# Performance work log

Hardware: AMD Instinct MI355X
Metric: run time of the kernel (lower is better)

Reference implementation:

```python
import jax, jax.numpy as jnp
import numpy as np

# Config (matches init_kwargs)
B, T_IN, N, F_IN = 64, 12, 500, 2
N_RES, N_DIL, N_SKIP, N_END = 64, 64, 256, 512
K_SIZE, N_BLOCKS, N_LAYERS = 2, 4, 2
EDGE_DIM, N_PRED, N_OUT = 2, 12, 1
RECEPTIVE = N_BLOCKS * (K_SIZE - 1) * (2 ** N_LAYERS - 1) + 1  # 13
DILS = [2 ** i for _ in range(N_BLOCKS) for i in range(N_LAYERS)]  # [1,2,1,2,1,2,1,2]
L = len(DILS)
BN_EPS = 1e-5


def setup_inputs() -> dict:
    key = jax.random.key(0)
    ks = jax.random.split(key, 20)
    inputs = jax.random.normal(ks[0], (B, T_IN, N, F_IN), dtype=jnp.float32)
    u = jax.random.uniform(ks[1], (EDGE_DIM, N, N), dtype=jnp.float32)
    supports = u / u.sum(-1, keepdims=True)  # row-stochastic diffusion matrices
    def w(k, shape, fan_in):
        return jax.random.normal(k, shape, dtype=jnp.float32) * (1.0 / np.sqrt(fan_in))
    return {
        "inputs": inputs,
        "supports": supports,
        "enter_w": w(ks[2], (N_RES, F_IN), F_IN),
        "enter_b": jnp.zeros((N_RES,), jnp.float32),
        "filter_w": w(ks[3], (L, N_DIL, N_RES, 1, K_SIZE), N_RES * K_SIZE),
        "filter_b": jnp.zeros((L, N_DIL), jnp.float32),
        "gate_w": w(ks[4], (L, N_DIL, N_RES, 1, K_SIZE), N_RES * K_SIZE),
        "gate_b": jnp.zeros((L, N_DIL), jnp.float32),
        "gconv_w": w(ks[5], (L, N_RES, EDGE_DIM * N_DIL), EDGE_DIM * N_DIL),
        "gconv_b": jnp.zeros((L, N_RES), jnp.float32),
        "skip_w": w(ks[6], (L, N_SKIP, N_DIL), N_DIL),
        "skip_b": jnp.zeros((L, N_SKIP), jnp.float32),
        "bn_gamma": jnp.ones((L, N_RES), jnp.float32),
        "bn_beta": jnp.zeros((L, N_RES), jnp.float32),
        "out1_w": w(ks[7], (N_END, N_SKIP), N_SKIP),
        "out1_b": jnp.zeros((N_END,), jnp.float32),
        "out2_w": w(ks[8], (N_PRED * N_OUT, N_END), N_END),
        "out2_b": jnp.zeros((N_PRED * N_OUT,), jnp.float32),
    }


def _conv_t(x, w, b, dil):
    # x: [B,C,N,T], w: [O,I,1,k] dilated along time, VALID padding
    y = jax.lax.conv_general_dilated(x, w, window_strides=(1, 1), padding="VALID",
                                     rhs_dilation=(1, dil),
                                     dimension_numbers=("NCHW", "OIHW", "NCHW"))
    return y + b[None, :, None, None]


def _forward(inputs, supports, enter_w, enter_b, filter_w, filter_b, gate_w, gate_b,
             gconv_w, gconv_b, skip_w, skip_b, bn_gamma, bn_beta,
             out1_w, out1_b, out2_w, out2_b):
    x = jnp.transpose(inputs, (0, 3, 2, 1))  # [B,F,N,T]
    pad = RECEPTIVE - x.shape[3]
    if pad > 0:
        x = jnp.pad(x, ((0, 0), (0, 0), (0, 0), (pad, 0)))
    x = jnp.einsum("of,bfnt->bont", enter_w, x) + enter_b[None, :, None, None]
    b = x.shape[0]
    skip = jnp.zeros((b, N_SKIP, N, x.shape[3]), jnp.float32)
    for i, d in enumerate(DILS):
        residual = x
        f = jnp.tanh(_conv_t(residual, filter_w[i], filter_b[i], d))
        g = jax.nn.sigmoid(_conv_t(residual, gate_w[i], gate_b[i], d))
        x = f * g  # [B, n_dil, N, t']
        s = jnp.einsum("oc,bcnt->bont", skip_w[i], x) + skip_b[i][None, :, None, None]
        skip = skip[..., -s.shape[3]:] + s
        # graph diffusion conv: propagate over each support, mix channels
        h = jnp.einsum("knm,bcmt->bkcnt", supports, x)
        bb, kk, cc, nn, tt = h.shape
        h = h.reshape(bb, kk * cc, nn, tt)
        x = jnp.einsum("oi,bint->bont", gconv_w[i], h) + gconv_b[i][None, :, None, None]
        # dropout is identity in eval mode
        x = x + residual[..., -x.shape[3]:]
        # BatchNorm2d (training-mode batch statistics)
        mean = x.mean(axis=(0, 2, 3), keepdims=True)
        var = ((x - mean) ** 2).mean(axis=(0, 2, 3), keepdims=True)
        x = (x - mean) * jax.lax.rsqrt(var + BN_EPS)
        x = x * bn_gamma[i][None, :, None, None] + bn_beta[i][None, :, None, None]
    y = jax.nn.relu(skip)  # [B, n_skips, N, 1]
    y = jax.nn.relu(jnp.einsum("os,bsnt->bont", out1_w, y) + out1_b[None, :, None, None])
    y = jnp.einsum("oe,bent->bont", out2_w, y) + out2_b[None, :, None, None]
    # [B, n_pred*n_out, N, 1] -> [B, n_pred, N, n_out]
    y = y.reshape(b, N_PRED, -1, N)
    return jnp.swapaxes(y, -1, -2)


def reference(inputs, supports, enter_w, enter_b, filter_w, filter_b, gate_w, gate_b,
              gconv_w, gconv_b, skip_w, skip_b, bn_gamma, bn_beta,
              out1_w, out1_b, out2_w, out2_b):
    return _forward(inputs, supports, enter_w, enter_b, filter_w, filter_b, gate_w, gate_b,
                    gconv_w, gconv_b, skip_w, skip_b, bn_gamma, bn_beta,
                    out1_w, out1_b, out2_w, out2_b)
```

## Files before the change

kernel.cpp:

```cpp
#include <hip/hip_runtime.h>

typedef float v4 __attribute__((ext_vector_type(4)));
typedef short bf8 __attribute__((ext_vector_type(8)));
typedef unsigned short u16;
typedef unsigned int u32;

#define DEVI __device__ __forceinline__

namespace {

constexpr int B = 64, C = 64, NPT = 500, NP = 512, T0 = 13, SC = 256, EC = 512, PR = 12;
constexpr size_t SLOTP = (size_t)B * C * NP;

constexpr size_t SZ_BUF  = 13 * SLOTP * 2;
constexpr size_t OFF_SK  = 2 * SZ_BUF;
constexpr size_t SZ_SK   = (size_t)SC * B * NPT * 4;
constexpr size_t OFF_ST  = OFF_SK + SZ_SK;
constexpr size_t OFF_STP = OFF_ST + 1024;
constexpr size_t OFF_W1T = OFF_STP + 1024;
constexpr size_t OFF_WMX = OFF_W1T + (size_t)131072*4;
constexpr size_t OFF_WFB = OFF_WMX + (size_t)65536*2;
constexpr size_t OFF_WGB = OFF_WFB + (size_t)65536*2;
constexpr size_t OFF_SWB = OFF_WGB + (size_t)65536*2;
constexpr size_t OFF_SPD = OFF_SWB + (size_t)131072*2;
constexpr size_t OFF_PSUM = OFF_SPD + (size_t)524288*2;
constexpr size_t WS_NEED = OFF_PSUM + (size_t)768*128*4;

DEVI float sigm(float x) { return 1.f / (1.f + expf(-x)); }
DEVI float bf2f(u16 u) { u32 x = ((u32)u) << 16; float f; __builtin_memcpy(&f, &x, 4); return f; }
DEVI u16 f2bf(float f) { u32 x; __builtin_memcpy(&x, &f, 4); return (u16)((x + 0x7FFF + ((x >> 16) & 1)) >> 16); }
DEVI int swzA(int n, int k) { int byte = (n << 8) + (k << 1); byte ^= (((n >> 1) ^ (n >> 3)) & 7) << 4; return byte; }
DEVI int swzS(int n, int cp) { int byte = (n << 7) + (cp << 1); byte ^= (((n >> 1) ^ (n >> 3)) & 7) << 4; return byte; }
DEVI int swzX(int r, int c) { int byte = (r << 10) + (c << 1); byte ^= (r & 7) << 4; return byte; }
DEVI int swzG(int n, int k) { int byte = (n << 7) + (k << 1); byte ^= (n & 7) << 4; return byte; }

__global__ void k_debug_ws(float* __restrict__ out, float val) {
  int i = blockIdx.x * 256 + threadIdx.x;
  if (i < B * PR * NPT) out[i] = val;
}

__global__ void k_prep(const float* __restrict__ fw, const float* __restrict__ gw,
                       const float* __restrict__ sw, const float* __restrict__ gcw,
                       const float* __restrict__ o1w, const float* __restrict__ sup,
                       u16* __restrict__ WFB, u16* __restrict__ WGB,
                       u16* __restrict__ SWB, u16* __restrict__ WMX,
                       float* __restrict__ W1T, u16* __restrict__ SPD,
                       float* __restrict__ STP) {
  int i = blockIdx.x * 256 + threadIdx.x;
  if (i < 65536) {
    int k = i & 127, cp = (i >> 7) & 63, l = i >> 13;
    int tap = k >> 6, c = k & 63;
    int g = ((l * 64 + cp) * 64 + c) * 2 + tap;
    WFB[i] = f2bf(fw[g]);
    WGB[i] = f2bf(gw[g]);
  }
  int j = i - 65536;
  if (j >= 0 && j < 131072) {
    int c = j & 63, o = (j >> 6) & 255, l = j >> 14;
    SWB[j] = f2bf(sw[(l * 256 + o) * 64 + c]);
  }
  int k2 = i - 196608;
  if (k2 >= 0 && k2 < 65536) WMX[k2] = f2bf(gcw[k2]);
  int m = i - 262144;
  if (m >= 0 && m < 131072) {
    int e = m & 511, o = m >> 9;
    W1T[m] = o1w[e * 256 + o];
  }
  int sp = i - 393216;
  if (sp >= 0 && sp < 524288) {
    int mm = sp & 511, n = (sp >> 9) & 511, s = sp >> 18;
    float v = (n < NPT && mm < NPT) ? sup[(size_t)s * NPT * NPT + (size_t)n * NPT + mm] : 0.f;
    SPD[sp] = f2bf(v);
  }
  int q = i - 917504;
  if (q >= 0 && q < 192) STP[q] = (q >= 64 && q < 128) ? 1.f : 0.f;
}

__global__ void k_enter(const float* __restrict__ in, const float* __restrict__ ew,
                        const float* __restrict__ eb, u16* __restrict__ X) {
  size_t idx = (size_t)blockIdx.x * 256 + threadIdx.x;
  if (idx >= 13 * SLOTP) return;
  int t = (int)(idx / SLOTP);
  size_t r = idx % SLOTP;
  int n = (int)(r % NP);
  int c = (int)((r / NP) % C);
  int b = (int)(r / ((size_t)NP * C));
  float v = 0.f;
  if (n < NPT) {
    v = eb[c];
    if (t > 0) {
      const float* ip = in + (((size_t)b * 12 + (t - 1)) * NPT + n) * 2;
      v += ew[c * 2] * ip[0] + ew[c * 2 + 1] * ip[1];
    }
  }
  X[idx] = f2bf(v);
}

__global__ void k_zero_sk(float* __restrict__ p) {
  size_t i = ((size_t)blockIdx.x * 256 + threadIdx.x) * 4;
  v4 z = {};
  *(v4*)&p[i] = z;
}

__global__ __launch_bounds__(1024) void k_gatedconv(
    const u16* __restrict__ X, u16* __restrict__ XA,
    const float* __restrict__ STP,
    const u16* __restrict__ WFl, const float* __restrict__ bfb,
    const u16* __restrict__ WGl, const float* __restrict__ bgb,
    const u16* __restrict__ SWl, const float* __restrict__ sb,
    float* __restrict__ SK, int d, int Tp) {
  __shared__ u16 L[65536];
  const int lane = threadIdx.x, w = threadIdx.y;
  const int tid = w * 64 + lane;
  const int t = blockIdx.x, b = blockIdx.y;
  const int lrow = lane & 15, kgrp = lane >> 4;
  const int nbase = w * 32;

  for (int i = tid; i < 8192; i += 1024) {
    int tap = i >> 12;
    int c = (i >> 6) & 63;
    int n0 = (i & 63) * 8;
    const u16* src = &X[(size_t)(t + tap * d) * SLOTP + ((size_t)b * C + c) * NP + n0];
    float mean = STP[c], scl = STP[64 + c], sh = STP[128 + c];
    ushort4 a = *(const ushort4*)src;
    ushort4 a2 = *(const ushort4*)(src + 4);
    u16 vals[8] = {a.x, a.y, a.z, a.w, a2.x, a2.y, a2.z, a2.w};
    int k = tap * 64 + c;
#pragma unroll
    for (int jj = 0; jj < 8; ++jj) {
      int n = n0 + jj;
      L[swzA(n, k) >> 1] = f2bf((bf2f(vals[jj]) - mean) * scl + sh);
    }
  }
  __syncthreads();

  v4 af[2][4], ag[2][4];
#pragma unroll
  for (int a1 = 0; a1 < 2; ++a1)
#pragma unroll
    for (int a2 = 0; a2 < 4; ++a2) { af[a1][a2] = (v4){0.f,0.f,0.f,0.f}; ag[a1][a2] = (v4){0.f,0.f,0.f,0.f}; }

#pragma unroll
  for (int k0 = 0; k0 < 128; k0 += 32) {
    const int kof = k0 + kgrp * 8;
    bf8 Av[2];
#pragma unroll
    for (int nt = 0; nt < 2; ++nt) {
      int n = nbase + nt * 16 + lrow;
      Av[nt] = *(const bf8*)&L[swzA(n, kof) >> 1];
    }
#pragma unroll
    for (int ct = 0; ct < 4; ++ct) {
      bf8 Fw = *(const bf8*)&WFl[(size_t)(ct * 16 + lrow) * 128 + kof];
      bf8 Gw = *(const bf8*)&WGl[(size_t)(ct * 16 + lrow) * 128 + kof];
#pragma unroll
      for (int nt = 0; nt < 2; ++nt) {
        af[nt][ct] = __builtin_amdgcn_mfma_f32_16x16x32_bf16(Av[nt], Fw, af[nt][ct], 0, 0, 0);
        ag[nt][ct] = __builtin_amdgcn_mfma_f32_16x16x32_bf16(Av[nt], Gw, ag[nt][ct], 0, 0, 0);
      }
    }
  }

  const size_t xab = (size_t)t * SLOTP + (size_t)b * C * NP;
  ushort4 ovv[2][4];
#pragma unroll
  for (int nt = 0; nt < 2; ++nt) {
    int n0s = nbase + nt * 16 + kgrp * 4;
#pragma unroll
    for (int ct = 0; ct < 4; ++ct) {
      int cp = ct * 16 + lrow;
      float fb = bfb[cp], gb2 = bgb[cp];
      ushort4 ov;
      ov.x = f2bf(tanhf(af[nt][ct][0] + fb) * sigm(ag[nt][ct][0] + gb2));
      ov.y = f2bf(tanhf(af[nt][ct][1] + fb) * sigm(ag[nt][ct][1] + gb2));
      ov.z = f2bf(tanhf(af[nt][ct][2] + fb) * sigm(ag[nt][ct][2] + gb2));
      ov.w = f2bf(tanhf(af[nt][ct][3] + fb) * sigm(ag[nt][ct][3] + gb2));
      ovv[nt][ct] = ov;
      if (n0s < NPT) *(ushort4*)&XA[xab + (size_t)cp * NP + n0s] = ov;
    }
  }

  if (t == Tp - 1) {
    __syncthreads();
#pragma unroll
    for (int nt = 0; nt < 2; ++nt) {
      int n0s = nbase + nt * 16 + kgrp * 4;
#pragma unroll
      for (int ct = 0; ct < 4; ++ct) {
        int cp = ct * 16 + lrow;
        ushort4 ov = ovv[nt][ct];
        L[swzS(n0s + 0, cp) >> 1] = ov.x;
        L[swzS(n0s + 1, cp) >> 1] = ov.y;
        L[swzS(n0s + 2, cp) >> 1] = ov.z;
        L[swzS(n0s + 3, cp) >> 1] = ov.w;
      }
    }
    __syncthreads();
#pragma unroll 1
    for (int ot = 0; ot < 16; ++ot) {
      v4 a[2];
#pragma unroll
      for (int nt = 0; nt < 2; ++nt) a[nt] = (v4){0.f,0.f,0.f,0.f};
#pragma unroll
      for (int k0 = 0; k0 < 64; k0 += 32) {
        const int kof = k0 + kgrp * 8;
        bf8 Bs = *(const bf8*)&SWl[(size_t)(ot * 16 + lrow) * 64 + kof];
#pragma unroll
        for (int nt = 0; nt < 2; ++nt) {
          int n = nbase + nt * 16 + lrow;
          bf8 Av2 = *(const bf8*)&L[swzS(n, kof) >> 1];
          a[nt] = __builtin_amdgcn_mfma_f32_16x16x32_bf16(Av2, Bs, a[nt], 0, 0, 0);
        }
      }
      int o = ot * 16 + lrow;
      float bb = sb[o];
#pragma unroll
      for (int nt = 0; nt < 2; ++nt) {
        int n0s = nbase + nt * 16 + kgrp * 4;
        if (n0s < NPT) {
          float* dst = &SK[(size_t)o * (B * NPT) + (size_t)b * NPT + n0s];
          v4 old = *(const v4*)dst;
          *(v4*)dst = old + a[nt] + bb;
        }
      }
    }
  }
}

__global__ __launch_bounds__(512) void k_diffmix(
    const u16* __restrict__ XA, const u16* __restrict__ XIN, u16* __restrict__ XOUT,
    const u16* __restrict__ SPD, const u16* __restrict__ WMXl,
    const float* __restrict__ gb, const float* __restrict__ STP,
    float* __restrict__ PSUM, int d) {
  __shared__ u16 SH[65536];
  __shared__ float sst[128];
  u16* XS = SH;
  u16* GS = SH + 32768;
  const int lane = threadIdx.x;
  const int w = threadIdx.y;
  const int tid = w * 64 + lane;
  const int t = blockIdx.x, b = blockIdx.y;
  const int lrow = lane & 15;
  const int kgrp = lane >> 4;
  const int nbase = w * 64;
  const size_t xabase = ((size_t)t * (B * C) + (size_t)b * C) * NP;
  if (tid < 128) sst[tid] = 0.f;

  for (int i = tid; i < 4096; i += 512) {
    int c = i >> 6, slot = i & 63;
    const u16* src = &XA[xabase + (size_t)c * NP + slot * 8];
    ushort4 a0 = *(const ushort4*)src;
    ushort4 a1 = *(const ushort4*)(src + 4);
    int byte = swzX(c, slot * 8);
    *(ushort4*)&XS[byte >> 1] = a0;
    *(ushort4*)&XS[(byte >> 1) + 4] = a1;
  }
  __syncthreads();

  v4 acc2[4][4];
#pragma unroll
  for (int a = 0; a < 4; ++a)
#pragma unroll
    for (int c2 = 0; c2 < 4; ++c2) acc2[a][c2] = (v4){0.f, 0.f, 0.f, 0.f};

#pragma unroll 1
  for (int s = 0; s < 2; ++s) {
    v4 acc[4][4];
#pragma unroll
    for (int a = 0; a < 4; ++a)
#pragma unroll
      for (int c2 = 0; c2 < 4; ++c2) acc[a][c2] = (v4){0.f, 0.f, 0.f, 0.f};
    const u16* Sb = SPD + (size_t)s * (512 * 512);
    bf8 Ac[4];
#pragma unroll
    for (int nt = 0; nt < 4; ++nt)
      Ac[nt] = *(const bf8*)&Sb[(size_t)(nbase + nt * 16 + lrow) * 512 + kgrp * 8];
#pragma unroll 1
    for (int k0 = 0; k0 < 512; k0 += 32) {
      const int kof = k0 + kgrp * 8;
      bf8 An[4];
      if (k0 + 32 < 512) {
#pragma unroll
        for (int nt = 0; nt < 4; ++nt)
          An[nt] = *(const bf8*)&Sb[(size_t)(nbase + nt * 16 + lrow) * 512 + kof + 32];
      }
      bf8 Bf[4];
#pragma unroll
      for (int ct = 0; ct < 4; ++ct)
        Bf[ct] = *(const bf8*)&XS[swzX(ct * 16 + lrow, kof) >> 1];
#pragma unroll
      for (int nt = 0; nt < 4; ++nt)
#pragma unroll
        for (int ct = 0; ct < 4; ++ct)
          acc[nt][ct] = __builtin_amdgcn_mfma_f32_16x16x32_bf16(Ac[nt], Bf[ct], acc[nt][ct], 0, 0, 0);
#pragma unroll
      for (int nt = 0; nt < 4; ++nt) Ac[nt] = An[nt];
    }
#pragma unroll
    for (int nt = 0; nt < 4; ++nt)
#pragma unroll
      for (int ct = 0; ct < 4; ++ct)
#pragma unroll
        for (int r = 0; r < 4; ++r) {
          int n = nbase + nt * 16 + kgrp * 4 + r;
          int k = ct * 16 + lrow;
          GS[swzG(n, k) >> 1] = f2bf(acc[nt][ct][r]);
        }
    __syncthreads();
#pragma unroll
    for (int k0 = 0; k0 < 64; k0 += 32) {
      const int kof = k0 + kgrp * 8;
      bf8 Af[4], Bw[4];
#pragma unroll
      for (int nt = 0; nt < 4; ++nt)
        Af[nt] = *(const bf8*)&GS[swzG(nbase + nt * 16 + lrow, kof) >> 1];
#pragma unroll
      for (int ot = 0; ot < 4; ++ot)
        Bw[ot] = *(const bf8*)&WMXl[(size_t)(ot * 16 + lrow) * 128 + s * 64 + kof];
#pragma unroll
      for (int nt = 0; nt < 4; ++nt)
#pragma unroll
        for (int ot = 0; ot < 4; ++ot)
          acc2[nt][ot] = __builtin_amdgcn_mfma_f32_16x16x32_bf16(Af[nt], Bw[ot], acc2[nt][ot], 0, 0, 0);
    }
    __syncthreads();
  }

#pragma unroll
  for (int nt = 0; nt < 4; ++nt) {
    int n0 = nbase + nt * 16 + kgrp * 4;
#pragma unroll
    for (int ot = 0; ot < 4; ++ot) {
      int o = ot * 16 + lrow;
      int byte = swzX(o, n0);
      ushort4 gv;
      gv.x = f2bf(acc2[nt][ot][0]);
      gv.y = f2bf(acc2[nt][ot][1]);
      gv.z = f2bf(acc2[nt][ot][2]);
      gv.w = f2bf(acc2[nt][ot][3]);
      *(ushort4*)&XS[byte >> 1] = gv;
    }
  }
  __syncthreads();
  const size_t rbase = ((size_t)(t + d) * (B * C) + (size_t)b * C) * NP;
#pragma unroll 1
  for (int i = 0; i < 8; ++i) {
    int idx = i * 512 + tid;
    int o = idx >> 6;
    int ck = idx & 63;
    int byte = swzX(o, ck * 8);
    ushort4 g0 = *(const ushort4*)&XS[byte >> 1];
    ushort4 g1 = *(const ushort4*)&XS[(byte >> 1) + 4];
    int n0 = ck * 8;
    const u16* rp = &XIN[rbase + (size_t)o * NP + n0];
    ushort4 r0 = *(const ushort4*)rp;
    ushort4 r1 = *(const ushort4*)(rp + 4);
    float m = STP[o], sc = STP[64 + o], h = STP[128 + o];
    float bias = gb[o];
    float v[8];
    v[0] = bf2f(g0.x) + bias + (bf2f(r0.x) - m) * sc + h;
    v[1] = bf2f(g0.y) + bias + (bf2f(r0.y) - m) * sc + h;
    v[2] = bf2f(g0.z) + bias + (bf2f(r0.z) - m) * sc + h;
    v[3] = bf2f(g0.w) + bias + (bf2f(r0.w) - m) * sc + h;
    v[4] = bf2f(g1.x) + bias + (bf2f(r1.x) - m) * sc + h;
    v[5] = bf2f(g1.y) + bias + (bf2f(r1.y) - m) * sc + h;
    v[6] = bf2f(g1.z) + bias + (bf2f(r1.z) - m) * sc + h;
    v[7] = bf2f(g1.w) + bias + (bf2f(r1.w) - m) * sc + h;
    ushort4 s0, s1;
    s0.x = f2bf(v[0]); s0.y = f2bf(v[1]); s0.z = f2bf(v[2]); s0.w = f2bf(v[3]);
    s1.x = f2bf(v[4]); s1.y = f2bf(v[5]); s1.z = f2bf(v[6]); s1.w = f2bf(v[7]);
    u16* op = &XOUT[xabase + (size_t)o * NP + n0];
    *(ushort4*)op = s0;
    *(ushort4*)(op + 4) = s1;
    float ls = 0.f, lq = 0.f;
#pragma unroll
    for (int e = 0; e < 8; ++e)
      if (n0 + e < NPT) { ls += v[e]; lq += v[e] * v[e]; }
#pragma unroll
    for (int off = 32; off; off >>= 1) {
      ls += __shfl_down(ls, off, 64);
      lq += __shfl_down(lq, off, 64);
    }
    if (lane == 0) {
      atomicAdd(&sst[o], ls);
      atomicAdd(&sst[64 + o], lq);
    }
  }
  __syncthreads();
  if (tid < 128) PSUM[(size_t)(blockIdx.y * gridDim.x + blockIdx.x) * 128 + tid] = sst[tid];
}

__global__ __launch_bounds__(1024) void k_bnfin(
    const float* __restrict__ PSUM, float* __restrict__ stp,
    const float* __restrict__ gamma, const float* __restrict__ beta,
    int nblk, int Tp) {
  __shared__ double red[1024];
  int tid = threadIdx.x;
  int c = tid & 127;
  int ch = tid >> 7;
  double s = 0.0;
  for (int r = ch; r < nblk; r += 8) s += (double)PSUM[(size_t)r * 128 + c];
  red[tid] = s;
  __syncthreads();
  if (ch < 4) red[tid] += red[tid + 512];
  __syncthreads();
  if (ch < 2) red[tid] += red[tid + 256];
  __syncthreads();
  if (ch == 0) red[c] = red[c] + red[c + 128];
  __syncthreads();
  if (tid < 64) {
    double cnt = (double)Tp * (double)(B * NPT);
    double m = red[tid] / cnt;
    double v = red[64 + tid] / cnt - m * m;
    stp[tid] = (float)m;
    stp[64 + tid] = gamma[tid] * rsqrtf((float)v + 1e-5f);
    stp[128 + tid] = beta[tid];
  }
}

__global__ __launch_bounds__(256) void k_out1(const float* __restrict__ SK,
                                              const float* __restrict__ W1T,
                                              const float* __restrict__ b1,
                                              u16* __restrict__ H1) {
  __shared__ __align__(16) float ssm[32 * 64];
  __shared__ __align__(16) float wsm[32 * 64];
  const int tx = threadIdx.x, ty = threadIdx.y;
  const int tid = ty * 16 + tx;
  const int p0 = blockIdx.x * 64, e0 = blockIdx.y * 64;
  v4 acc[4] = {};
  for (int o0 = 0; o0 < SC; o0 += 32) {
    __syncthreads();
    for (int i = tid; i < 2048; i += 256) {
      int pp = i & 63, kk = i >> 6;
      ssm[i] = fmaxf(SK[(size_t)(o0 + kk) * (B * NPT) + p0 + pp], 0.f);
      wsm[i] = W1T[(size_t)(o0 + kk) * 512 + e0 + pp];
    }
    __syncthreads();
#pragma unroll
    for (int kk = 0; kk < 32; ++kk) {
      v4 sv = *(const v4*)&ssm[kk * 64 + tx * 4];
      v4 wv = *(const v4*)&wsm[kk * 64 + ty * 4];
#pragma unroll
      for (int r = 0; r < 4; ++r) acc[r] += wv[r] * sv;
    }
  }
#pragma unroll
  for (int r = 0; r < 4; ++r) {
    int e = e0 + ty * 4 + r;
    float bb = b1[e];
    size_t ob = (size_t)e * (B * NPT) + p0 + tx * 4;
#pragma unroll
    for (int q = 0; q < 4; ++q) H1[ob + q] = f2bf(fmaxf(acc[r][q] + bb, 0.f));
  }
}

__global__ __launch_bounds__(256) void k_out2(const u16* __restrict__ H1,
                                              const float* __restrict__ W2,
                                              const float* __restrict__ b2,
                                              float* __restrict__ out) {
  int idx = blockIdx.x * 256 + threadIdx.x;
  if (idx >= B * PR * NPT) return;
  int n = idx % NPT;
  int p12 = (idx / NPT) % PR;
  int b = idx / (NPT * PR);
  size_t p = (size_t)b * NPT + n;
  const float* w = W2 + p12 * EC;
  float acc = b2[p12];
  for (int e = 0; e < EC; e += 4) {
    acc += w[e] * bf2f(H1[(size_t)e * (B * NPT) + p])
         + w[e + 1] * bf2f(H1[(size_t)(e + 1) * (B * NPT) + p])
         + w[e + 2] * bf2f(H1[(size_t)(e + 2) * (B * NPT) + p])
         + w[e + 3] * bf2f(H1[(size_t)(e + 3) * (B * NPT) + p]);
  }
  out[idx] = acc;
}

}

extern "C" void kernel_launch(void* const* d_in, const int* in_sizes, int n_in,
                              void* d_out, int out_size, void* d_ws, size_t ws_size,
                              hipStream_t stream) {
  const float* inputs  = (const float*)d_in[0];
  const float* sup     = (const float*)d_in[1];
  const float* enter_w = (const float*)d_in[2];
  const float* enter_b = (const float*)d_in[3];
  const float* filt_w  = (const float*)d_in[4];
  const float* filt_b  = (const float*)d_in[5];
  const float* gate_w  = (const float*)d_in[6];
  const float* gate_b  = (const float*)d_in[7];
  const float* gconv_w = (const float*)d_in[8];
  const float* gconv_b = (const float*)d_in[9];
  const float* skip_w  = (const float*)d_in[10];
  const float* skip_b  = (const float*)d_in[11];
  const float* bn_g    = (const float*)d_in[12];
  const float* bn_b    = (const float*)d_in[13];
  const float* o1w     = (const float*)d_in[14];
  const float* o1b     = (const float*)d_in[15];
  const float* o2w     = (const float*)d_in[16];
  const float* o2b     = (const float*)d_in[17];
  (void)in_sizes; (void)n_in; (void)out_size;

  if (ws_size < WS_NEED) {
    k_debug_ws<<<1500, 256, 0, stream>>>((float*)d_out, (float)(ws_size >> 20));
    return;
  }

  char* base = (char*)d_ws;
  u16*    buf0 = (u16*)base;
  u16*    buf1 = (u16*)(base + SZ_BUF);
  float*  SK   = (float*)(base + OFF_SK);
  float*  STP  = (float*)(base + OFF_STP);
  float*  W1T  = (float*)(base + OFF_W1T);
  u16*    WMX  = (u16*)(base + OFF_WMX);
  u16*    WFB  = (u16*)(base + OFF_WFB);
  u16*    WGB  = (u16*)(base + OFF_WGB);
  u16*    SWB  = (u16*)(base + OFF_SWB);
  u16*    SPD  = (u16*)(base + OFF_SPD);
  float*  PSUM = (float*)(base + OFF_PSUM);

  k_prep<<<3586, 256, 0, stream>>>(filt_w, gate_w, skip_w, gconv_w, o1w, sup,
                                   WFB, WGB, SWB, WMX, W1T, SPD, STP);
  k_enter<<<(int)((13 * SLOTP) / 256), 256, 0, stream>>>(inputs, enter_w, enter_b, buf0);
  k_zero_sk<<<8000, 256, 0, stream>>>(SK);

  static const int dils[8] = {1, 2, 1, 2, 1, 2, 1, 2};
  u16* bufs[2] = {buf0, buf1};
  int T = T0;
  for (int l = 0; l < 8; ++l) {
    const int d = dils[l];
    const int Tp = T - d;
    u16* XIN = bufs[l & 1];
    u16* XAb = bufs[(l + 1) & 1];
    k_gatedconv<<<dim3(Tp, B), dim3(64, 16), 0, stream>>>(
        XIN, XAb, STP, WFB + l * 8192, filt_b + l * 64, WGB + l * 8192, gate_b + l * 64,
        SWB + l * 16384, skip_b + l * 256, SK, d, Tp);
    if (l < 7) {
      k_diffmix<<<dim3(Tp, B), dim3(64, 8), 0, stream>>>(
          XAb, XIN, XAb, SPD, WMX + l * 8192, gconv_b + l * 64, STP, PSUM, d);
      k_bnfin<<<1, 1024, 0, stream>>>(PSUM, STP, bn_g + l * 64, bn_b + l * 64, Tp * B, Tp);
    }
    T = Tp;
  }

  u16* H1 = buf1;
  k_out1<<<dim3(500, 8), dim3(16, 16), 0, stream>>>(SK, W1T, o1b, H1);
  k_out2<<<1500, 256, 0, stream>>>(H1, o2w, o2b, (float*)d_out);
}
```

Measured before the change: 2.138 ms.

## Fuse gated conv into diffusion-mix kernel, fold BatchNorm into next layer weights

```diff
diff --git a/kernel.cpp b/kernel.cpp
--- a/kernel.cpp
+++ b/kernel.cpp
@@ -24,13 +24,15 @@
 constexpr size_t OFF_SWB = OFF_WGB + (size_t)65536*2;
 constexpr size_t OFF_SPD = OFF_SWB + (size_t)131072*2;
 constexpr size_t OFF_PSUM = OFF_SPD + (size_t)524288*2;
-constexpr size_t WS_NEED = OFF_PSUM + (size_t)768*128*4;
+constexpr size_t OFF_WFP = OFF_PSUM + (size_t)768*128*4;
+constexpr size_t OFF_WGP = OFF_WFP + 16384;
+constexpr size_t OFF_BFP = OFF_WGP + 16384;
+constexpr size_t OFF_BGP = OFF_BFP + 256;
+constexpr size_t WS_NEED = OFF_BGP + 256;
 
 DEVI float sigm(float x) { return 1.f / (1.f + expf(-x)); }
 DEVI float bf2f(u16 u) { u32 x = ((u32)u) << 16; float f; __builtin_memcpy(&f, &x, 4); return f; }
 DEVI u16 f2bf(float f) { u32 x; __builtin_memcpy(&x, &f, 4); return (u16)((x + 0x7FFF + ((x >> 16) & 1)) >> 16); }
-DEVI int swzA(int n, int k) { int byte = (n << 8) + (k << 1); byte ^= (((n >> 1) ^ (n >> 3)) & 7) << 4; return byte; }
-DEVI int swzS(int n, int cp) { int byte = (n << 7) + (cp << 1); byte ^= (((n >> 1) ^ (n >> 3)) & 7) << 4; return byte; }
 DEVI int swzX(int r, int c) { int byte = (r << 10) + (c << 1); byte ^= (r & 7) << 4; return byte; }
 DEVI int swzG(int n, int k) { int byte = (n << 7) + (k << 1); byte ^= (n & 7) << 4; return byte; }
 
@@ -42,10 +44,13 @@
 __global__ void k_prep(const float* __restrict__ fw, const float* __restrict__ gw,
                        const float* __restrict__ sw, const float* __restrict__ gcw,
                        const float* __restrict__ o1w, const float* __restrict__ sup,
+                       const float* __restrict__ fbias, const float* __restrict__ gbias,
                        u16* __restrict__ WFB, u16* __restrict__ WGB,
                        u16* __restrict__ SWB, u16* __restrict__ WMX,
                        float* __restrict__ W1T, u16* __restrict__ SPD,
-                       float* __restrict__ STP) {
+                       float* __restrict__ STP,
+                       u16* __restrict__ WFP, u16* __restrict__ WGP,
+                       float* __restrict__ BFP, float* __restrict__ BGP) {
   int i = blockIdx.x * 256 + threadIdx.x;
   if (i < 65536) {
     int k = i & 127, cp = (i >> 7) & 63, l = i >> 13;
@@ -74,6 +79,19 @@
   }
   int q = i - 917504;
   if (q >= 0 && q < 192) STP[q] = (q >= 64 && q < 128) ? 1.f : 0.f;
+  int w0 = i - 917696;
+  if (w0 >= 0 && w0 < 8192) {
+    int k = w0 & 127, cp = w0 >> 7;
+    int tap = k >> 6, c = k & 63;
+    int g = (cp * 64 + c) * 2 + tap;
+    WFP[w0] = f2bf(fw[g]);
+    WGP[w0] = f2bf(gw[g]);
+  }
+  int b0 = i - 925888;
+  if (b0 >= 0 && b0 < 128) {
+    if (b0 < 64) BFP[b0] = fbias[b0];
+    else BGP[b0 - 64] = gbias[b0 - 64];
+  }
 }
 
 __global__ void k_enter(const float* __restrict__ in, const float* __restrict__ ew,
@@ -82,9 +100,9 @@
   if (idx >= 13 * SLOTP) return;
   int t = (int)(idx / SLOTP);
   size_t r = idx % SLOTP;
-  int n = (int)(r % NP);
-  int c = (int)((r / NP) % C);
-  int b = (int)(r / ((size_t)NP * C));
+  int c = (int)(r & 63);
+  int n = (int)((r >> 6) & 511);
+  int b = (int)(r >> 15);
   float v = 0.f;
   if (n < NPT) {
     v = eb[c];
@@ -102,136 +120,15 @@
   *(v4*)&p[i] = z;
 }
 
-__global__ __launch_bounds__(1024) void k_gatedconv(
-    const u16* __restrict__ X, u16* __restrict__ XA,
-    const float* __restrict__ STP,
-    const u16* __restrict__ WFl, const float* __restrict__ bfb,
-    const u16* __restrict__ WGl, const float* __restrict__ bgb,
-    const u16* __restrict__ SWl, const float* __restrict__ sb,
-    float* __restrict__ SK, int d, int Tp) {
-  __shared__ u16 L[65536];
-  const int lane = threadIdx.x, w = threadIdx.y;
-  const int tid = w * 64 + lane;
-  const int t = blockIdx.x, b = blockIdx.y;
-  const int lrow = lane & 15, kgrp = lane >> 4;
-  const int nbase = w * 32;
-
-  for (int i = tid; i < 8192; i += 1024) {
-    int tap = i >> 12;
-    int c = (i >> 6) & 63;
-    int n0 = (i & 63) * 8;
-    const u16* src = &X[(size_t)(t + tap * d) * SLOTP + ((size_t)b * C + c) * NP + n0];
-    float mean = STP[c], scl = STP[64 + c], sh = STP[128 + c];
-    ushort4 a = *(const ushort4*)src;
-    ushort4 a2 = *(const ushort4*)(src + 4);
-    u16 vals[8] = {a.x, a.y, a.z, a.w, a2.x, a2.y, a2.z, a2.w};
-    int k = tap * 64 + c;
-#pragma unroll
-    for (int jj = 0; jj < 8; ++jj) {
-      int n = n0 + jj;
-      L[swzA(n, k) >> 1] = f2bf((bf2f(vals[jj]) - mean) * scl + sh);
-    }
-  }
-  __syncthreads();
-
-  v4 af[2][4], ag[2][4];
-#pragma unroll
-  for (int a1 = 0; a1 < 2; ++a1)
-#pragma unroll
-    for (int a2 = 0; a2 < 4; ++a2) { af[a1][a2] = (v4){0.f,0.f,0.f,0.f}; ag[a1][a2] = (v4){0.f,0.f,0.f,0.f}; }
-
-#pragma unroll
-  for (int k0 = 0; k0 < 128; k0 += 32) {
-    const int kof = k0 + kgrp * 8;
-    bf8 Av[2];
-#pragma unroll
-    for (int nt = 0; nt < 2; ++nt) {
-      int n = nbase + nt * 16 + lrow;
-      Av[nt] = *(const bf8*)&L[swzA(n, kof) >> 1];
-    }
-#pragma unroll
-    for (int ct = 0; ct < 4; ++ct) {
-      bf8 Fw = *(const bf8*)&WFl[(size_t)(ct * 16 + lrow) * 128 + kof];
-      bf8 Gw = *(const bf8*)&WGl[(size_t)(ct * 16 + lrow) * 128 + kof];
-#pragma unroll
-      for (int nt = 0; nt < 2; ++nt) {
-        af[nt][ct] = __builtin_amdgcn_mfma_f32_16x16x32_bf16(Av[nt], Fw, af[nt][ct], 0, 0, 0);
-        ag[nt][ct] = __builtin_amdgcn_mfma_f32_16x16x32_bf16(Av[nt], Gw, ag[nt][ct], 0, 0, 0);
-      }
-    }
-  }
-
-  const size_t xab = (size_t)t * SLOTP + (size_t)b * C * NP;
-  ushort4 ovv[2][4];
-#pragma unroll
-  for (int nt = 0; nt < 2; ++nt) {
-    int n0s = nbase + nt * 16 + kgrp * 4;
-#pragma unroll
-    for (int ct = 0; ct < 4; ++ct) {
-      int cp = ct * 16 + lrow;
-      float fb = bfb[cp], gb2 = bgb[cp];
-      ushort4 ov;
-      ov.x = f2bf(tanhf(af[nt][ct][0] + fb) * sigm(ag[nt][ct][0] + gb2));
-      ov.y = f2bf(tanhf(af[nt][ct][1] + fb) * sigm(ag[nt][ct][1] + gb2));
-      ov.z = f2bf(tanhf(af[nt][ct][2] + fb) * sigm(ag[nt][ct][2] + gb2));
-      ov.w = f2bf(tanhf(af[nt][ct][3] + fb) * sigm(ag[nt][ct][3] + gb2));
-      ovv[nt][ct] = ov;
-      if (n0s < NPT) *(ushort4*)&XA[xab + (size_t)cp * NP + n0s] = ov;
-    }
-  }
-
-  if (t == Tp - 1) {
-    __syncthreads();
-#pragma unroll
-    for (int nt = 0; nt < 2; ++nt) {
-      int n0s = nbase + nt * 16 + kgrp * 4;
-#pragma unroll
-      for (int ct = 0; ct < 4; ++ct) {
-        int cp = ct * 16 + lrow;
-        ushort4 ov = ovv[nt][ct];
-        L[swzS(n0s + 0, cp) >> 1] = ov.x;
-        L[swzS(n0s + 1, cp) >> 1] = ov.y;
-        L[swzS(n0s + 2, cp) >> 1] = ov.z;
-        L[swzS(n0s + 3, cp) >> 1] = ov.w;
-      }
-    }
-    __syncthreads();
-#pragma unroll 1
-    for (int ot = 0; ot < 16; ++ot) {
-      v4 a[2];
-#pragma unroll
-      for (int nt = 0; nt < 2; ++nt) a[nt] = (v4){0.f,0.f,0.f,0.f};
-#pragma unroll
-      for (int k0 = 0; k0 < 64; k0 += 32) {
-        const int kof = k0 + kgrp * 8;
-        bf8 Bs = *(const bf8*)&SWl[(size_t)(ot * 16 + lrow) * 64 + kof];
-#pragma unroll
-        for (int nt = 0; nt < 2; ++nt) {
-          int n = nbase + nt * 16 + lrow;
-          bf8 Av2 = *(const bf8*)&L[swzS(n, kof) >> 1];
-          a[nt] = __builtin_amdgcn_mfma_f32_16x16x32_bf16(Av2, Bs, a[nt], 0, 0, 0);
-        }
-      }
-      int o = ot * 16 + lrow;
-      float bb = sb[o];
-#pragma unroll
-      for (int nt = 0; nt < 2; ++nt) {
-        int n0s = nbase + nt * 16 + kgrp * 4;
-        if (n0s < NPT) {
-          float* dst = &SK[(size_t)o * (B * NPT) + (size_t)b * NPT + n0s];
-          v4 old = *(const v4*)dst;
-          *(v4*)dst = old + a[nt] + bb;
-        }
-      }
-    }
-  }
-}
-
-__global__ __launch_bounds__(512) void k_diffmix(
-    const u16* __restrict__ XA, const u16* __restrict__ XIN, u16* __restrict__ XOUT,
-    const u16* __restrict__ SPD, const u16* __restrict__ WMXl,
-    const float* __restrict__ gb, const float* __restrict__ STP,
-    float* __restrict__ PSUM, int d) {
+__global__ __launch_bounds__(512) void k_fused(
+    const u16* __restrict__ XIN, u16* __restrict__ XOUT,
+    const u16* __restrict__ SPD,
+    const u16* __restrict__ WFP, const float* __restrict__ BFP,
+    const u16* __restrict__ WGP, const float* __restrict__ BGP,
+    const u16* __restrict__ SWl, const float* __restrict__ sb, float* __restrict__ SK,
+    const u16* __restrict__ WMXl, const float* __restrict__ gb,
+    const float* __restrict__ STP, float* __restrict__ PSUM,
+    int d, int Tp, int dodiff) {
   __shared__ u16 SH[65536];
   __shared__ float sst[128];
   u16* XS = SH;
@@ -243,19 +140,95 @@
   const int lrow = lane & 15;
   const int kgrp = lane >> 4;
   const int nbase = w * 64;
-  const size_t xabase = ((size_t)t * (B * C) + (size_t)b * C) * NP;
+  const size_t x_t  = (size_t)t * SLOTP + (size_t)b * NP * C;
+  const size_t x_td = (size_t)(t + d) * SLOTP + (size_t)b * NP * C;
   if (tid < 128) sst[tid] = 0.f;
 
-  for (int i = tid; i < 4096; i += 512) {
-    int c = i >> 6, slot = i & 63;
-    const u16* src = &XA[xabase + (size_t)c * NP + slot * 8];
-    ushort4 a0 = *(const ushort4*)src;
-    ushort4 a1 = *(const ushort4*)(src + 4);
-    int byte = swzX(c, slot * 8);
-    *(ushort4*)&XS[byte >> 1] = a0;
-    *(ushort4*)&XS[(byte >> 1) + 4] = a1;
-  }
-  __syncthreads();
+  v4 af[4][4], ag[4][4];
+#pragma unroll
+  for (int a1 = 0; a1 < 4; ++a1)
+#pragma unroll
+    for (int a2 = 0; a2 < 4; ++a2) { af[a1][a2] = (v4){0.f,0.f,0.f,0.f}; ag[a1][a2] = (v4){0.f,0.f,0.f,0.f}; }
+#pragma unroll
+  for (int k0 = 0; k0 < 128; k0 += 32) {
+    const int kof = k0 + kgrp * 8;
+    const int tap = kof >> 6, coff = kof & 63;
+    const u16* xsl = XIN + (tap ? x_td : x_t);
+    bf8 Av[4];
+#pragma unroll
+    for (int nt = 0; nt < 4; ++nt) {
+      int n = nbase + nt * 16 + lrow;
+      Av[nt] = *(const bf8*)&xsl[(size_t)n * C + coff];
+    }
+#pragma unroll
+    for (int ct = 0; ct < 4; ++ct) {
+      bf8 Fw = *(const bf8*)&WFP[(ct * 16 + lrow) * 128 + kof];
+      bf8 Gw = *(const bf8*)&WGP[(ct * 16 + lrow) * 128 + kof];
+#pragma unroll
+      for (int nt = 0; nt < 4; ++nt) {
+        af[nt][ct] = __builtin_amdgcn_mfma_f32_16x16x32_bf16(Av[nt], Fw, af[nt][ct], 0, 0, 0);
+        ag[nt][ct] = __builtin_amdgcn_mfma_f32_16x16x32_bf16(Av[nt], Gw, ag[nt][ct], 0, 0, 0);
+      }
+    }
+  }
+#pragma unroll
+  for (int nt = 0; nt < 4; ++nt) {
+    int n0s = nbase + nt * 16 + kgrp * 4;
+#pragma unroll
+    for (int ct = 0; ct < 4; ++ct) {
+      int cp = ct * 16 + lrow;
+      float fb = BFP[cp], gb2 = BGP[cp];
+      ushort4 ov;
+      ov.x = f2bf(tanhf(af[nt][ct][0] + fb) * sigm(ag[nt][ct][0] + gb2));
+      ov.y = f2bf(tanhf(af[nt][ct][1] + fb) * sigm(ag[nt][ct][1] + gb2));
+      ov.z = f2bf(tanhf(af[nt][ct][2] + fb) * sigm(ag[nt][ct][2] + gb2));
+      ov.w = f2bf(tanhf(af[nt][ct][3] + fb) * sigm(ag[nt][ct][3] + gb2));
+      *(ushort4*)&XS[swzX(cp, n0s) >> 1] = ov;
+    }
+  }
+  __syncthreads();
+
+  if (t == Tp - 1) {
+    bf8 Bsf[4][2];
+#pragma unroll
+    for (int nt = 0; nt < 4; ++nt)
+#pragma unroll
+      for (int kk = 0; kk < 2; ++kk) {
+        int n = nbase + nt * 16 + lrow;
+        bf8 v;
+#pragma unroll
+        for (int e = 0; e < 8; ++e) {
+          int c = kk * 32 + kgrp * 8 + e;
+          v[e] = (short)XS[swzX(c, n) >> 1];
+        }
+        Bsf[nt][kk] = v;
+      }
+#pragma unroll 1
+    for (int ot = 0; ot < 16; ++ot) {
+      v4 a[4];
+#pragma unroll
+      for (int nt = 0; nt < 4; ++nt) a[nt] = (v4){0.f,0.f,0.f,0.f};
+#pragma unroll
+      for (int kk = 0; kk < 2; ++kk) {
+        bf8 Aw = *(const bf8*)&SWl[(size_t)(ot * 16 + lrow) * 64 + kk * 32 + kgrp * 8];
+#pragma unroll
+        for (int nt = 0; nt < 4; ++nt)
+          a[nt] = __builtin_amdgcn_mfma_f32_16x16x32_bf16(Bsf[nt][kk], Aw, a[nt], 0, 0, 0);
+      }
+      int o = ot * 16 + lrow;
+      float bb = sb[o];
+#pragma unroll
+      for (int nt = 0; nt < 4; ++nt) {
+        int n0s = nbase + nt * 16 + kgrp * 4;
+        if (n0s < NPT) {
+          float* dst = &SK[(size_t)o * (B * NPT) + (size_t)b * NPT + n0s];
+          v4 old = *(const v4*)dst;
+          *(v4*)dst = old + a[nt] + bb;
+        }
+      }
+    }
+  }
+  if (!dodiff) return;
 
   v4 acc2[4][4];
 #pragma unroll
@@ -327,63 +300,72 @@
   }
 
 #pragma unroll
-  for (int nt = 0; nt < 4; ++nt) {
-    int n0 = nbase + nt * 16 + kgrp * 4;
+  for (int nt = 0; nt < 4; ++nt)
 #pragma unroll
     for (int ot = 0; ot < 4; ++ot) {
       int o = ot * 16 + lrow;
-      int byte = swzX(o, n0);
-      ushort4 gv;
-      gv.x = f2bf(acc2[nt][ot][0]);
-      gv.y = f2bf(acc2[nt][ot][1]);
-      gv.z = f2bf(acc2[nt][ot][2]);
-      gv.w = f2bf(acc2[nt][ot][3]);
-      *(ushort4*)&XS[byte >> 1] = gv;
-    }
-  }
-  __syncthreads();
-  const size_t rbase = ((size_t)(t + d) * (B * C) + (size_t)b * C) * NP;
+#pragma unroll
+      for (int r = 0; r < 4; ++r) {
+        int n = nbase + nt * 16 + kgrp * 4 + r;
+        GS[swzG(n, o) >> 1] = f2bf(acc2[nt][ot][r]);
+      }
+    }
+  __syncthreads();
+
+  const int cchunk = tid & 7;
+  const int c0 = cchunk * 8;
+  float m8[8], sc8[8], h8[8], gb8[8];
+#pragma unroll
+  for (int e = 0; e < 8; ++e) {
+    m8[e] = STP[c0 + e];
+    sc8[e] = STP[64 + c0 + e];
+    h8[e] = STP[128 + c0 + e];
+    gb8[e] = gb[c0 + e];
+  }
+  float s8[8] = {}, q8[8] = {};
 #pragma unroll 1
   for (int i = 0; i < 8; ++i) {
     int idx = i * 512 + tid;
-    int o = idx >> 6;
-    int ck = idx & 63;
-    int byte = swzX(o, ck * 8);
-    ushort4 g0 = *(const ushort4*)&XS[byte >> 1];
-    ushort4 g1 = *(const ushort4*)&XS[(byte >> 1) + 4];
-    int n0 = ck * 8;
-    const u16* rp = &XIN[rbase + (size_t)o * NP + n0];
+    int n = idx >> 3;
+    int byte = swzG(n, c0);
+    ushort4 g0 = *(const ushort4*)&GS[byte >> 1];
+    ushort4 g1 = *(const ushort4*)&GS[(byte >> 1) + 4];
+    const u16* rp = &XIN[x_td + (size_t)n * C + c0];
     ushort4 r0 = *(const ushort4*)rp;
     ushort4 r1 = *(const ushort4*)(rp + 4);
-    float m = STP[o], sc = STP[64 + o], h = STP[128 + o];
-    float bias = gb[o];
     float v[8];
-    v[0] = bf2f(g0.x) + bias + (bf2f(r0.x) - m) * sc + h;
-    v[1] = bf2f(g0.y) + bias + (bf2f(r0.y) - m) * sc + h;
-    v[2] = bf2f(g0.z) + bias + (bf2f(r0.z) - m) * sc + h;
-    v[3] = bf2f(g0.w) + bias + (bf2f(r0.w) - m) * sc + h;
-    v[4] = bf2f(g1.x) + bias + (bf2f(r1.x) - m) * sc + h;
-    v[5] = bf2f(g1.y) + bias + (bf2f(r1.y) - m) * sc + h;
-    v[6] = bf2f(g1.z) + bias + (bf2f(r1.z) - m) * sc + h;
-    v[7] = bf2f(g1.w) + bias + (bf2f(r1.w) - m) * sc + h;
+    v[0] = bf2f(g0.x) + gb8[0] + (bf2f(r0.x) - m8[0]) * sc8[0] + h8[0];
+    v[1] = bf2f(g0.y) + gb8[1] + (bf2f(r0.y) - m8[1]) * sc8[1] + h8[1];
+    v[2] = bf2f(g0.z) + gb8[2] + (bf2f(r0.z) - m8[2]) * sc8[2] + h8[2];
+    v[3] = bf2f(g0.w) + gb8[3] + (bf2f(r0.w) - m8[3]) * sc8[3] + h8[3];
+    v[4] = bf2f(g1.x) + gb8[4] + (bf2f(r1.x) - m8[4]) * sc8[4] + h8[4];
+    v[5] = bf2f(g1.y) + gb8[5] + (bf2f(r1.y) - m8[5]) * sc8[5] + h8[5];
+    v[6] = bf2f(g1.z) + gb8[6] + (bf2f(r1.z) - m8[6]) * sc8[6] + h8[6];
+    v[7] = bf2f(g1.w) + gb8[7] + (bf2f(r1.w) - m8[7]) * sc8[7] + h8[7];
     ushort4 s0, s1;
     s0.x = f2bf(v[0]); s0.y = f2bf(v[1]); s0.z = f2bf(v[2]); s0.w = f2bf(v[3]);
     s1.x = f2bf(v[4]); s1.y = f2bf(v[5]); s1.z = f2bf(v[6]); s1.w = f2bf(v[7]);
-    u16* op = &XOUT[xabase + (size_t)o * NP + n0];
+    u16* op = &XOUT[x_t + (size_t)n * C + c0];
     *(ushort4*)op = s0;
     *(ushort4*)(op + 4) = s1;
-    float ls = 0.f, lq = 0.f;
-#pragma unroll
-    for (int e = 0; e < 8; ++e)
-      if (n0 + e < NPT) { ls += v[e]; lq += v[e] * v[e]; }
-#pragma unroll
-    for (int off = 32; off; off >>= 1) {
-      ls += __shfl_down(ls, off, 64);
-      lq += __shfl_down(lq, off, 64);
-    }
-    if (lane == 0) {
-      atomicAdd(&sst[o], ls);
-      atomicAdd(&sst[64 + o], lq);
+    if (n < NPT) {
+#pragma unroll
+      for (int e = 0; e < 8; ++e) { s8[e] += v[e]; q8[e] += v[e] * v[e]; }
+    }
+  }
+#pragma unroll
+  for (int off = 8; off < 64; off <<= 1) {
+#pragma unroll
+    for (int e = 0; e < 8; ++e) {
+      s8[e] += __shfl_xor(s8[e], off, 64);
+      q8[e] += __shfl_xor(q8[e], off, 64);
+    }
+  }
+  if (lane < 8) {
+#pragma unroll
+    for (int e = 0; e < 8; ++e) {
+      atomicAdd(&sst[c0 + e], s8[e]);
+      atomicAdd(&sst[64 + c0 + e], q8[e]);
     }
   }
   __syncthreads();
@@ -393,8 +375,13 @@
 __global__ __launch_bounds__(1024) void k_bnfin(
     const float* __restrict__ PSUM, float* __restrict__ stp,
     const float* __restrict__ gamma, const float* __restrict__ beta,
+    const u16* __restrict__ WFB_nl, const u16* __restrict__ WGB_nl,
+    const float* __restrict__ fb_nl, const float* __restrict__ gb_nl,
+    u16* __restrict__ WFP, u16* __restrict__ WGP,
+    float* __restrict__ BFP, float* __restrict__ BGP,
     int nblk, int Tp) {
   __shared__ double red[1024];
+  __shared__ float sscl[64], sshm[64];
   int tid = threadIdx.x;
   int c = tid & 127;
   int ch = tid >> 7;
@@ -412,9 +399,28 @@
     double cnt = (double)Tp * (double)(B * NPT);
     double m = red[tid] / cnt;
     double v = red[64 + tid] / cnt - m * m;
-    stp[tid] = (float)m;
-    stp[64 + tid] = gamma[tid] * rsqrtf((float)v + 1e-5f);
+    float mf = (float)m;
+    float scl = gamma[tid] * rsqrtf((float)v + 1e-5f);
+    stp[tid] = mf;
+    stp[64 + tid] = scl;
     stp[128 + tid] = beta[tid];
+    sscl[tid] = scl;
+    sshm[tid] = beta[tid] - mf * scl;
+  }
+  __syncthreads();
+  for (int i = tid; i < 16384; i += 1024) {
+    int which = i >> 13, j = i & 8191;
+    int cc = j & 63;
+    float sc = sscl[cc];
+    if (which == 0) WFP[j] = f2bf(bf2f(WFB_nl[j]) * sc);
+    else            WGP[j] = f2bf(bf2f(WGB_nl[j]) * sc);
+  }
+  if (tid < 128) {
+    int cp = tid & 63;
+    const u16* W = (tid < 64) ? WFB_nl : WGB_nl;
+    float acc = (tid < 64) ? fb_nl[cp] : gb_nl[cp];
+    for (int k = 0; k < 128; ++k) acc += sshm[k & 63] * bf2f(W[cp * 128 + k]);
+    if (tid < 64) BFP[cp] = acc; else BGP[cp] = acc;
   }
 }
 
@@ -517,9 +523,15 @@
   u16*    SWB  = (u16*)(base + OFF_SWB);
   u16*    SPD  = (u16*)(base + OFF_SPD);
   float*  PSUM = (float*)(base + OFF_PSUM);
-
-  k_prep<<<3586, 256, 0, stream>>>(filt_w, gate_w, skip_w, gconv_w, o1w, sup,
-                                   WFB, WGB, SWB, WMX, W1T, SPD, STP);
+  u16*    WFP  = (u16*)(base + OFF_WFP);
+  u16*    WGP  = (u16*)(base + OFF_WGP);
+  float*  BFP  = (float*)(base + OFF_BFP);
+  float*  BGP  = (float*)(base + OFF_BGP);
+
+  k_prep<<<3618, 256, 0, stream>>>(filt_w, gate_w, skip_w, gconv_w, o1w, sup,
+                                   filt_b, gate_b,
+                                   WFB, WGB, SWB, WMX, W1T, SPD, STP,
+                                   WFP, WGP, BFP, BGP);
   k_enter<<<(int)((13 * SLOTP) / 256), 256, 0, stream>>>(inputs, enter_w, enter_b, buf0);
   k_zero_sk<<<8000, 256, 0, stream>>>(SK);
 
@@ -529,20 +541,23 @@
   for (int l = 0; l < 8; ++l) {
     const int d = dils[l];
     const int Tp = T - d;
-    u16* XIN = bufs[l & 1];
-    u16* XAb = bufs[(l + 1) & 1];
-    k_gatedconv<<<dim3(Tp, B), dim3(64, 16), 0, stream>>>(
-        XIN, XAb, STP, WFB + l * 8192, filt_b + l * 64, WGB + l * 8192, gate_b + l * 64,
-        SWB + l * 16384, skip_b + l * 256, SK, d, Tp);
+    u16* XIN  = bufs[l & 1];
+    u16* XOUT = bufs[(l + 1) & 1];
+    k_fused<<<dim3(Tp, B), dim3(64, 8), 0, stream>>>(
+        XIN, XOUT, SPD, WFP, BFP, WGP, BGP,
+        SWB + l * 16384, skip_b + l * 256, SK,
+        WMX + l * 8192, gconv_b + l * 64, STP, PSUM, d, Tp, l < 7 ? 1 : 0);
     if (l < 7) {
-      k_diffmix<<<dim3(Tp, B), dim3(64, 8), 0, stream>>>(
-          XAb, XIN, XAb, SPD, WMX + l * 8192, gconv_b + l * 64, STP, PSUM, d);
-      k_bnfin<<<1, 1024, 0, stream>>>(PSUM, STP, bn_g + l * 64, bn_b + l * 64, Tp * B, Tp);
+      k_bnfin<<<1, 1024, 0, stream>>>(
+          PSUM, STP, bn_g + l * 64, bn_b + l * 64,
+          WFB + (l + 1) * 8192, WGB + (l + 1) * 8192,
+          filt_b + (l + 1) * 64, gate_b + (l + 1) * 64,
+          WFP, WGP, BFP, BGP, Tp * B, Tp);
     }
     T = Tp;
   }
 
-  u16* H1 = buf1;
+  u16* H1 = buf0;
   k_out1<<<dim3(500, 8), dim3(16, 16), 0, stream>>>(SK, W1T, o1b, H1);
   k_out2<<<1500, 256, 0, stream>>>(H1, o2w, o2b, (float*)d_out);
 }
```

After: 1.954 ms. 1.09x faster.
